# Performance work log

Hardware: AMD Instinct MI355X
Metric: run time of the kernel (lower is better)

## Reference

```python
import jax, jax.numpy as jnp
import numpy as np

B, S, T, D = 4, 512, 512, 256


def setup_inputs() -> dict:
    key = jax.random.key(0)
    ks = jax.random.split(key, 10)
    scale = 1.0 / np.sqrt(D)
    return {
        "source": jax.random.normal(ks[0], (B, S, D), jnp.float32),
        "target": jax.random.normal(ks[1], (B, T, D), jnp.float32),
        "W_src": jax.random.uniform(ks[2], (D, D), jnp.float32, -scale, scale),
        "b_src": jax.random.uniform(ks[3], (D,), jnp.float32, -scale, scale),
        "W_tgt": jax.random.uniform(ks[4], (D, D), jnp.float32, -scale, scale),
        "b_tgt": jax.random.uniform(ks[5], (D,), jnp.float32, -scale, scale),
        "W_res": jax.random.uniform(ks[6], (D, 1), jnp.float32, -scale, scale),
        "b_res": jax.random.uniform(ks[7], (1,), jnp.float32, -scale, scale),
        "W_prob": jax.random.uniform(ks[8], (D, 2), jnp.float32, -scale, scale),
        "b_prob": jax.random.uniform(ks[9], (2,), jnp.float32, -scale, scale),
    }


def reference(source, target, W_src, b_src, W_tgt, b_tgt, W_res, b_res, W_prob, b_prob):
    # source: (B,S,D), target: (B,T,D)
    src_lin = jnp.einsum("bsd,de->bse", source, W_src) + b_src  # (B,S,D)
    tgt_lin = jnp.einsum("btd,de->bte", target, W_tgt) + b_tgt  # (B,T,D)
    # Bahdanau-style additive attention: (B,T,S,D) broadcast, tanh, D->1
    h = jnp.tanh(src_lin[:, None, :, :] + tgt_lin[:, :, None, :])  # (B,T,S,D)
    genP = jnp.einsum("btsd,d->bts", h, W_res[:, 0]) + b_res[0]     # (B,T,S)
    prob = jax.nn.softmax(jnp.einsum("btd,de->bte", target, W_prob) + b_prob, axis=-1)  # (B,T,2)
    return genP, prob
```

## Files before the change

### kernel.cpp

```cpp
#include <hip/hip_runtime.h>

#define B_ 4
#define S_ 512
#define T_ 512
#define D_ 256
#define NSRC (B_ * S_)
#define NROW 4096
#define K2F 2.8853900817779268f

typedef __attribute__((ext_vector_type(8))) short short8;
typedef __attribute__((ext_vector_type(4))) float f32x4;
typedef __attribute__((ext_vector_type(2))) float f32x2;

__device__ __forceinline__ unsigned short f2bf(float f) {
    union { float f; unsigned u; } v; v.f = f;
    unsigned r = v.u + 0x7FFF + ((v.u >> 16) & 1);
    return (unsigned short)(r >> 16);
}

__global__ __launch_bounds__(256) void ysyt_kernel(
    const float* __restrict__ src, const float* __restrict__ tgt,
    const float* __restrict__ Wsrc, const float* __restrict__ Wtgt,
    const float* __restrict__ Wp,  const float* __restrict__ bp,
    const float* __restrict__ bsrc, const float* __restrict__ btgt,
    float* __restrict__ yst, float* __restrict__ out)
{
    __shared__ unsigned short lwt[16384];
    const int bid = blockIdx.x, tid = threadIdx.x;
    const int lane = tid & 63, w = tid >> 6;

    if (bid < 256) {
        const int rowblk = bid >> 2, colq = bid & 3;
        const int R0 = rowblk * 64;
        const int n = lane & 15, quad = lane >> 4;
        const int mat = (R0 >= NSRC) ? 1 : 0;
        const float* bias = mat ? btgt : bsrc;
        const float* Wm = mat ? Wtgt : Wsrc;
        const float* xb = mat ? &tgt[(R0 - NSRC) * D_] : &src[R0 * D_];

        {
            const int r = tid;
            const int ksr = r >> 5, qr = (r >> 3) & 3, jr = r & 7;
            const int wbase = ksr * 512 + qr * 8 + jr;
            #pragma unroll 4
            for (int i = 0; i < 16; i++) {
                float4 v = *(const float4*)&Wm[r * D_ + colq * 64 + 4 * i];
                const int cc = 4 * i;
                lwt[((cc + 0) >> 4) * 4096 + ((cc + 0) & 15) * 32 + wbase] = f2bf(v.x);
                lwt[((cc + 1) >> 4) * 4096 + ((cc + 1) & 15) * 32 + wbase] = f2bf(v.y);
                lwt[((cc + 2) >> 4) * 4096 + ((cc + 2) & 15) * 32 + wbase] = f2bf(v.z);
                lwt[((cc + 3) >> 4) * 4096 + ((cc + 3) & 15) * 32 + wbase] = f2bf(v.w);
            }
        }

        short8 af[8];
        #pragma unroll
        for (int ks = 0; ks < 8; ks++) {
            const float* p = &xb[(w * 16 + n) * D_ + ks * 32 + quad * 8];
            float4 u0 = *(const float4*)p;
            float4 u1 = *(const float4*)(p + 4);
            short8 v;
            v[0] = (short)f2bf(u0.x); v[1] = (short)f2bf(u0.y);
            v[2] = (short)f2bf(u0.z); v[3] = (short)f2bf(u0.w);
            v[4] = (short)f2bf(u1.x); v[5] = (short)f2bf(u1.y);
            v[6] = (short)f2bf(u1.z); v[7] = (short)f2bf(u1.w);
            af[ks] = v;
        }
        __syncthreads();

        #pragma unroll
        for (int gc = 0; gc < 4; gc++) {
            const int gcol = colq * 4 + gc;
            const unsigned short* bp2 = &lwt[gc * 4096 + n * 32 + quad * 8];
            short8 bf[8];
            #pragma unroll
            for (int ks = 0; ks < 8; ks++) bf[ks] = *(const short8*)&bp2[ks * 512];
            f32x4 a4 = {0.f, 0.f, 0.f, 0.f};
            #pragma unroll
            for (int ks = 0; ks < 8; ks++)
                a4 = __builtin_amdgcn_mfma_f32_16x16x32_bf16(af[ks], bf[ks], a4, 0, 0, 0);
            const float bv = bias[gcol * 16 + n];
            float4 o;
            o.x = __builtin_amdgcn_exp2f((a4[0] + bv) * K2F);
            o.y = __builtin_amdgcn_exp2f((a4[1] + bv) * K2F);
            o.z = __builtin_amdgcn_exp2f((a4[2] + bv) * K2F);
            o.w = __builtin_amdgcn_exp2f((a4[3] + bv) * K2F);
            *(float4*)&yst[(gcol * 16 + n) * NROW + R0 + w * 16 + quad * 4] = o;
        }
    } else {
        int row  = (bid - 256) * 4 + w;
        float p0 = 0.f, p1 = 0.f;
        #pragma unroll
        for (int i = 0; i < 4; i++) {
            int d = lane + i * 64;
            float v = tgt[row * D_ + d];
            float2 wv = *(const float2*)&Wp[d * 2];
            p0 = fmaf(v, wv.x, p0);
            p1 = fmaf(v, wv.y, p1);
        }
        #pragma unroll
        for (int off = 32; off > 0; off >>= 1) {
            p0 += __shfl_down(p0, off, 64);
            p1 += __shfl_down(p1, off, 64);
        }
        if (lane == 0) {
            const float L2E = 1.4426950408889634f;
            float l0 = p0 + bp[0], l1 = p1 + bp[1];
            float e10 = __builtin_amdgcn_exp2f((l1 - l0) * L2E);
            float e01 = __builtin_amdgcn_exp2f((l0 - l1) * L2E);
            out[B_ * T_ * S_ + row * 2 + 0] = __builtin_amdgcn_rcpf(1.f + e10);
            out[B_ * T_ * S_ + row * 2 + 1] = __builtin_amdgcn_rcpf(1.f + e01);
        }
    }
}

#define CLS 36
__global__ __launch_bounds__(256) void genp_kernel(
    const float* __restrict__ yst,
    const float* __restrict__ Wres, const float* __restrict__ bres,
    float* __restrict__ out)
{
    __shared__ float lys[2][64][CLS];
    __shared__ float lyt[2][64][CLS];
    __shared__ float c0s;

    const int tid = threadIdx.x;
    const int lane = tid & 63, w = tid >> 6;
    const int s0 = blockIdx.x * 32;
    const int t0 = blockIdx.y * 32;
    const int b  = blockIdx.z;
    const int m = tid & 15;
    const int g = tid >> 4;
    const int r = tid >> 3;
    const int q = tid & 7;

    if (w == 0) {
        float s = Wres[lane] + Wres[lane + 64] + Wres[lane + 128] + Wres[lane + 192];
        #pragma unroll
        for (int off = 32; off > 0; off >>= 1) s += __shfl_xor(s, off, 64);
        if (lane == 0) c0s = s + bres[0];
    }

    const int ysbase = b * S_ + s0;
    const int ytbase = NSRC + b * T_ + t0;

    {
        float4 a0 = *(const float4*)&yst[(r)      * NROW + ysbase + 4 * q];
        float4 a1 = *(const float4*)&yst[(r + 32) * NROW + ysbase + 4 * q];
        float4 b0 = *(const float4*)&yst[(r)      * NROW + ytbase + 4 * q];
        float4 b1 = *(const float4*)&yst[(r + 32) * NROW + ytbase + 4 * q];
        *(float4*)&lys[0][r][4 * q]      = a0;
        *(float4*)&lys[0][r + 32][4 * q] = a1;
        *(float4*)&lyt[0][r][4 * q]      = b0;
        *(float4*)&lyt[0][r + 32][4 * q] = b1;
    }
    __syncthreads();

    f32x2 acc[2];
    acc[0] = (f32x2){0.f, 0.f};
    acc[1] = (f32x2){0.f, 0.f};
    const f32x2 one2 = {1.f, 1.f};

    for (int c = 0; c < 4; c++) {
        const int bi = c & 1;
        float4 pa0, pa1, pb0, pb1;
        if (c < 3) {
            const int dn = (c + 1) * 64;
            pa0 = *(const float4*)&yst[(dn + r)      * NROW + ysbase + 4 * q];
            pa1 = *(const float4*)&yst[(dn + r + 32) * NROW + ysbase + 4 * q];
            pb0 = *(const float4*)&yst[(dn + r)      * NROW + ytbase + 4 * q];
            pb1 = *(const float4*)&yst[(dn + r + 32) * NROW + ytbase + 4 * q];
        }

        const float* wp = &Wres[c * 64];
        #pragma unroll 2
        for (int kq = 0; kq < 8; kq++) {
            const int d0 = 8 * kq;
            f32x2 ap[8];
            float2 ct[8];
            f32x2 wv[8];
            #pragma unroll
            for (int k = 0; k < 8; k++) {
                float2 a2 = *(const float2*)&lys[bi][d0 + k][2 * m];
                ct[k] = *(const float2*)&lyt[bi][d0 + k][2 * g];
                ap[k] = (f32x2){a2.x, a2.y};
                const float wk = wp[d0 + k];
                wv[k] = (f32x2){wk, wk};
            }
            #pragma unroll
            for (int i = 0; i < 2; i++) {
                const float c0 = i ? ct[0].y : ct[0].x;
                f32x2 dd[8];
                #pragma unroll
                for (int k = 0; k < 8; k++) {
                    const float cv = i ? ct[k].y : ct[k].x;
                    const f32x2 cs = {cv, cv};
                    dd[k] = ap[k] * cs + one2;
                }
                f32x2 p01 = dd[0] * dd[1];
                f32x2 p23 = dd[2] * dd[3];
                f32x2 p45 = dd[4] * dd[5];
                f32x2 p67 = dd[6] * dd[7];
                f32x2 q03 = p01 * p23;
                f32x2 q47 = p45 * p67;
                f32x2 den = q03 * q47;
                f32x2 u01 = dd[1] * wv[0]; u01 = dd[0] * wv[1] + u01;
                f32x2 u23 = dd[3] * wv[2]; u23 = dd[2] * wv[3] + u23;
                f32x2 u45 = dd[5] * wv[4]; u45 = dd[4] * wv[5] + u45;
                f32x2 u67 = dd[7] * wv[6]; u67 = dd[6] * wv[7] + u67;
                f32x2 n03 = u01 * p23; n03 = u23 * p01 + n03;
                f32x2 n47 = u45 * p67; n47 = u67 * p45 + n47;
                f32x2 num = n03 * q47; num = n47 * q03 + num;
                f32x2 rr;
                rr.x = __builtin_amdgcn_rcpf(den.x);
                rr.y = __builtin_amdgcn_rcpf(den.y);
                acc[i] = num * rr + acc[i];
                (void)c0;
            }
        }

        if (c < 3) {
            *(float4*)&lys[bi ^ 1][r][4 * q]      = pa0;
            *(float4*)&lys[bi ^ 1][r + 32][4 * q] = pa1;
            *(float4*)&lyt[bi ^ 1][r][4 * q]      = pb0;
            *(float4*)&lyt[bi ^ 1][r + 32][4 * q] = pb1;
        }
        __syncthreads();
    }

    const float C0 = c0s;
    #pragma unroll
    for (int i = 0; i < 2; i++) {
        float2 o;
        o.x = C0 - 2.f * acc[i].x;
        o.y = C0 - 2.f * acc[i].y;
        *(float2*)&out[(b * T_ + t0 + 2 * g + i) * S_ + s0 + 2 * m] = o;
    }
}

extern "C" void kernel_launch(void* const* d_in, const int* in_sizes, int n_in,
                              void* d_out, int out_size, void* d_ws, size_t ws_size,
                              hipStream_t stream) {
    const float* source = (const float*)d_in[0];
    const float* target = (const float*)d_in[1];
    const float* W_src  = (const float*)d_in[2];
    const float* b_src  = (const float*)d_in[3];
    const float* W_tgt  = (const float*)d_in[4];
    const float* b_tgt  = (const float*)d_in[5];
    const float* W_res  = (const float*)d_in[6];
    const float* b_res  = (const float*)d_in[7];
    const float* W_prob = (const float*)d_in[8];
    const float* b_prob = (const float*)d_in[9];
    float* out = (float*)d_out;

    float* yst = (float*)d_ws;

    ysyt_kernel<<<768, 256, 0, stream>>>(source, target, W_src, W_tgt,
                                         W_prob, b_prob, b_src, b_tgt,
                                         yst, out);
    genp_kernel<<<dim3(16, 16, 4), 256, 0, stream>>>(yst, W_res, b_res, out);
}
```

Baseline: 105.5 us.

## Split genP reduction over D halves, drop LDS staging, accumulate via atomics

The genP kernel no longer stages yst tiles through double-buffered shared memory. Each thread now loads its source and target columns straight from global memory into registers, with software prefetch. The D dimension is split across two blocks per batch, so each block covers 64 sources by 32 targets over half of D, and partial sums are combined with atomic adds into the output. The rational tanh product now groups 4 terms instead of 8, which roughly doubles the reciprocal count per element. The atomic accumulation also relies on the output being zeroed beforehand, and nothing visible in the launch code does that.

```diff
diff --git a/kernel.cpp b/kernel.cpp
--- a/kernel.cpp
+++ b/kernel.cpp
@@ -114,127 +114,104 @@
     }
 }
 
-#define CLS 36
 __global__ __launch_bounds__(256) void genp_kernel(
     const float* __restrict__ yst,
     const float* __restrict__ Wres, const float* __restrict__ bres,
     float* __restrict__ out)
 {
-    __shared__ float lys[2][64][CLS];
-    __shared__ float lyt[2][64][CLS];
-    __shared__ float c0s;
-
     const int tid = threadIdx.x;
-    const int lane = tid & 63, w = tid >> 6;
-    const int s0 = blockIdx.x * 32;
+    const int lane = tid & 63;
+    const int s0 = blockIdx.x * 64;
     const int t0 = blockIdx.y * 32;
-    const int b  = blockIdx.z;
-    const int m = tid & 15;
-    const int g = tid >> 4;
-    const int r = tid >> 3;
-    const int q = tid & 7;
-
-    if (w == 0) {
-        float s = Wres[lane] + Wres[lane + 64] + Wres[lane + 128] + Wres[lane + 192];
-        #pragma unroll
-        for (int off = 32; off > 0; off >>= 1) s += __shfl_xor(s, off, 64);
-        if (lane == 0) c0s = s + bres[0];
+    const int b  = blockIdx.z >> 1;
+    const int dh = blockIdx.z & 1;
+    const int m  = tid & 15;
+    const int g  = tid >> 4;
+
+    const int scol = b * S_ + s0 + 4 * m;
+    const int tcol = NSRC + b * T_ + t0 + 2 * g;
+    const int dbase = dh * 128;
+
+    f32x2 acc[2][2];
+    acc[0][0] = (f32x2){0.f, 0.f}; acc[0][1] = (f32x2){0.f, 0.f};
+    acc[1][0] = (f32x2){0.f, 0.f}; acc[1][1] = (f32x2){0.f, 0.f};
+    const f32x2 one2 = {1.f, 1.f};
+
+    #define KQLOAD(AS, AT, DQ) do {                                          \
+        _Pragma("unroll")                                                    \
+        for (int k = 0; k < 4; k++) {                                        \
+            AS[k] = *(const float4*)&yst[(size_t)((DQ) + k) * NROW + scol];  \
+            AT[k] = *(const float2*)&yst[(size_t)((DQ) + k) * NROW + tcol];  \
+        }                                                                    \
+    } while (0)
+
+    #define KQBODY(AS, AT, DQ) do {                                          \
+        const float w0 = Wres[(DQ) + 0], w1 = Wres[(DQ) + 1];                \
+        const float w2 = Wres[(DQ) + 2], w3 = Wres[(DQ) + 3];                \
+        const f32x2 wv0 = {w0, w0}, wv1 = {w1, w1};                          \
+        const f32x2 wv2 = {w2, w2}, wv3 = {w3, w3};                          \
+        _Pragma("unroll")                                                    \
+        for (int i = 0; i < 2; i++) {                                        \
+            const float c0 = i ? AT[0].y : AT[0].x;                          \
+            const float c1 = i ? AT[1].y : AT[1].x;                          \
+            const float c2 = i ? AT[2].y : AT[2].x;                          \
+            const float c3 = i ? AT[3].y : AT[3].x;                          \
+            const f32x2 c0v = {c0, c0}, c1v = {c1, c1};                      \
+            const f32x2 c2v = {c2, c2}, c3v = {c3, c3};                      \
+            _Pragma("unroll")                                                \
+            for (int jp = 0; jp < 2; jp++) {                                 \
+                const f32x2 a0 = jp ? (f32x2){AS[0].z, AS[0].w}              \
+                                    : (f32x2){AS[0].x, AS[0].y};             \
+                const f32x2 a1 = jp ? (f32x2){AS[1].z, AS[1].w}              \
+                                    : (f32x2){AS[1].x, AS[1].y};             \
+                const f32x2 a2 = jp ? (f32x2){AS[2].z, AS[2].w}              \
+                                    : (f32x2){AS[2].x, AS[2].y};             \
+                const f32x2 a3 = jp ? (f32x2){AS[3].z, AS[3].w}              \
+                                    : (f32x2){AS[3].x, AS[3].y};             \
+                f32x2 dd0 = a0 * c0v + one2;                                 \
+                f32x2 dd1 = a1 * c1v + one2;                                 \
+                f32x2 dd2 = a2 * c2v + one2;                                 \
+                f32x2 dd3 = a3 * c3v + one2;                                 \
+                f32x2 p01 = dd0 * dd1;                                       \
+                f32x2 p23 = dd2 * dd3;                                       \
+                f32x2 den = p01 * p23;                                       \
+                f32x2 u01 = dd1 * wv0; u01 = dd0 * wv1 + u01;                \
+                f32x2 u23 = dd3 * wv2; u23 = dd2 * wv3 + u23;                \
+                f32x2 num = u01 * p23; num = u23 * p01 + num;                \
+                f32x2 r;                                                     \
+                r.x = __builtin_amdgcn_rcpf(den.x);                          \
+                r.y = __builtin_amdgcn_rcpf(den.y);                          \
+                acc[i][jp] = num * r + acc[i][jp];                           \
+            }                                                                \
+        }                                                                    \
+    } while (0)
+
+    float4 sA[4], sB[4];
+    float2 tA[4], tB[4];
+    KQLOAD(sA, tA, dbase);
+    for (int it = 0; it < 16; it++) {
+        const int dq = dbase + it * 8;
+        KQLOAD(sB, tB, dq + 4);
+        KQBODY(sA, tA, dq);
+        if (it < 15) KQLOAD(sA, tA, dq + 8);
+        KQBODY(sB, tB, dq + 4);
     }
-
-    const int ysbase = b * S_ + s0;
-    const int ytbase = NSRC + b * T_ + t0;
-
-    {
-        float4 a0 = *(const float4*)&yst[(r)      * NROW + ysbase + 4 * q];
-        float4 a1 = *(const float4*)&yst[(r + 32) * NROW + ysbase + 4 * q];
-        float4 b0 = *(const float4*)&yst[(r)      * NROW + ytbase + 4 * q];
-        float4 b1 = *(const float4*)&yst[(r + 32) * NROW + ytbase + 4 * q];
-        *(float4*)&lys[0][r][4 * q]      = a0;
-        *(float4*)&lys[0][r + 32][4 * q] = a1;
-        *(float4*)&lyt[0][r][4 * q]      = b0;
-        *(float4*)&lyt[0][r + 32][4 * q] = b1;
-    }
-    __syncthreads();
-
-    f32x2 acc[2];
-    acc[0] = (f32x2){0.f, 0.f};
-    acc[1] = (f32x2){0.f, 0.f};
-    const f32x2 one2 = {1.f, 1.f};
-
-    for (int c = 0; c < 4; c++) {
-        const int bi = c & 1;
-        float4 pa0, pa1, pb0, pb1;
-        if (c < 3) {
-            const int dn = (c + 1) * 64;
-            pa0 = *(const float4*)&yst[(dn + r)      * NROW + ysbase + 4 * q];
-            pa1 = *(const float4*)&yst[(dn + r + 32) * NROW + ysbase + 4 * q];
-            pb0 = *(const float4*)&yst[(dn + r)      * NROW + ytbase + 4 * q];
-            pb1 = *(const float4*)&yst[(dn + r + 32) * NROW + ytbase + 4 * q];
-        }
-
-        const float* wp = &Wres[c * 64];
-        #pragma unroll 2
-        for (int kq = 0; kq < 8; kq++) {
-            const int d0 = 8 * kq;
-            f32x2 ap[8];
-            float2 ct[8];
-            f32x2 wv[8];
-            #pragma unroll
-            for (int k = 0; k < 8; k++) {
-                float2 a2 = *(const float2*)&lys[bi][d0 + k][2 * m];
-                ct[k] = *(const float2*)&lyt[bi][d0 + k][2 * g];
-                ap[k] = (f32x2){a2.x, a2.y};
-                const float wk = wp[d0 + k];
-                wv[k] = (f32x2){wk, wk};
-            }
-            #pragma unroll
-            for (int i = 0; i < 2; i++) {
-                const float c0 = i ? ct[0].y : ct[0].x;
-                f32x2 dd[8];
-                #pragma unroll
-                for (int k = 0; k < 8; k++) {
-                    const float cv = i ? ct[k].y : ct[k].x;
-                    const f32x2 cs = {cv, cv};
-                    dd[k] = ap[k] * cs + one2;
-                }
-                f32x2 p01 = dd[0] * dd[1];
-                f32x2 p23 = dd[2] * dd[3];
-                f32x2 p45 = dd[4] * dd[5];
-                f32x2 p67 = dd[6] * dd[7];
-                f32x2 q03 = p01 * p23;
-                f32x2 q47 = p45 * p67;
-                f32x2 den = q03 * q47;
-                f32x2 u01 = dd[1] * wv[0]; u01 = dd[0] * wv[1] + u01;
-                f32x2 u23 = dd[3] * wv[2]; u23 = dd[2] * wv[3] + u23;
-                f32x2 u45 = dd[5] * wv[4]; u45 = dd[4] * wv[5] + u45;
-                f32x2 u67 = dd[7] * wv[6]; u67 = dd[6] * wv[7] + u67;
-                f32x2 n03 = u01 * p23; n03 = u23 * p01 + n03;
-                f32x2 n47 = u45 * p67; n47 = u67 * p45 + n47;
-                f32x2 num = n03 * q47; num = n47 * q03 + num;
-                f32x2 rr;
-                rr.x = __builtin_amdgcn_rcpf(den.x);
-                rr.y = __builtin_amdgcn_rcpf(den.y);
-                acc[i] = num * rr + acc[i];
-                (void)c0;
-            }
-        }
-
-        if (c < 3) {
-            *(float4*)&lys[bi ^ 1][r][4 * q]      = pa0;
-            *(float4*)&lys[bi ^ 1][r + 32][4 * q] = pa1;
-            *(float4*)&lyt[bi ^ 1][r][4 * q]      = pb0;
-            *(float4*)&lyt[bi ^ 1][r + 32][4 * q] = pb1;
-        }
-        __syncthreads();
-    }
-
-    const float C0 = c0s;
+    #undef KQLOAD
+    #undef KQBODY
+
+    float cw = Wres[lane] + Wres[lane + 64] + Wres[lane + 128] + Wres[lane + 192];
+    #pragma unroll
+    for (int off = 32; off > 0; off >>= 1) cw += __shfl_xor(cw, off, 64);
+    const float C0 = (dh == 0) ? (cw + bres[0]) : 0.f;
+
     #pragma unroll
     for (int i = 0; i < 2; i++) {
-        float2 o;
-        o.x = C0 - 2.f * acc[i].x;
-        o.y = C0 - 2.f * acc[i].y;
-        *(float2*)&out[(b * T_ + t0 + 2 * g + i) * S_ + s0 + 2 * m] = o;
+        float* orow = &out[(size_t)(b * T_ + t0 + 2 * g + i) * S_ + s0 + 4 * m];
+        #pragma unroll
+        for (int jp = 0; jp < 2; jp++) {
+            unsafeAtomicAdd(&orow[2 * jp + 0], C0 - 2.f * acc[i][jp].x);
+            unsafeAtomicAdd(&orow[2 * jp + 1], C0 - 2.f * acc[i][jp].y);
+        }
     }
 }
 
@@ -258,5 +235,5 @@
     ysyt_kernel<<<768, 256, 0, stream>>>(source, target, W_src, W_tgt,
                                          W_prob, b_prob, b_src, b_tgt,
                                          yst, out);
-    genp_kernel<<<dim3(16, 16, 4), 256, 0, stream>>>(yst, W_res, b_res, out);
-}
+    genp_kernel<<<dim3(8, 16, 8), 256, 0, stream>>>(yst, W_res, b_res, out);
+}
```

Result: slower. 130.2 us (+23.4%).

## Store projected exponentials as row-major fp16 and read them as half8 in genp

Applied to the files above, without the earlier changes.

The projection kernel now stages its exp outputs in LDS, clamps them to 60000, converts them to fp16 and writes them row-major (row, D) instead of column-major fp32. The genp kernel loads half8 vectors along D, halving intermediate traffic and LDS footprint. It also remaps its thread-to-output tiling so that each thread handles rows m/m+16 and g/g+16. The risks are precision loss from fp16 storage and the clamp, plus an extra LDS pass and sync in the producer.

```diff
diff --git a/kernel.cpp b/kernel.cpp
--- a/kernel.cpp
+++ b/kernel.cpp
@@ -9,6 +9,7 @@
 #define K2F 2.8853900817779268f
 
 typedef __attribute__((ext_vector_type(8))) short short8;
+typedef __attribute__((ext_vector_type(8))) _Float16 half8;
 typedef __attribute__((ext_vector_type(4))) float f32x4;
 typedef __attribute__((ext_vector_type(2))) float f32x2;
 
@@ -23,9 +24,10 @@
     const float* __restrict__ Wsrc, const float* __restrict__ Wtgt,
     const float* __restrict__ Wp,  const float* __restrict__ bp,
     const float* __restrict__ bsrc, const float* __restrict__ btgt,
-    float* __restrict__ yst, float* __restrict__ out)
+    _Float16* __restrict__ ytr, float* __restrict__ out)
 {
     __shared__ unsigned short lwt[16384];
+    __shared__ _Float16 ltb[64][72];
     const int bid = blockIdx.x, tid = threadIdx.x;
     const int lane = tid & 63, w = tid >> 6;
 
@@ -80,12 +82,21 @@
             for (int ks = 0; ks < 8; ks++)
                 a4 = __builtin_amdgcn_mfma_f32_16x16x32_bf16(af[ks], bf[ks], a4, 0, 0, 0);
             const float bv = bias[gcol * 16 + n];
-            float4 o;
-            o.x = __builtin_amdgcn_exp2f((a4[0] + bv) * K2F);
-            o.y = __builtin_amdgcn_exp2f((a4[1] + bv) * K2F);
-            o.z = __builtin_amdgcn_exp2f((a4[2] + bv) * K2F);
-            o.w = __builtin_amdgcn_exp2f((a4[3] + bv) * K2F);
-            *(float4*)&yst[(gcol * 16 + n) * NROW + R0 + w * 16 + quad * 4] = o;
+            const int rl = w * 16 + quad * 4;
+            const int dl = gc * 16 + n;
+            ltb[rl + 0][dl] = (_Float16)fminf(__builtin_amdgcn_exp2f((a4[0] + bv) * K2F), 60000.f);
+            ltb[rl + 1][dl] = (_Float16)fminf(__builtin_amdgcn_exp2f((a4[1] + bv) * K2F), 60000.f);
+            ltb[rl + 2][dl] = (_Float16)fminf(__builtin_amdgcn_exp2f((a4[2] + bv) * K2F), 60000.f);
+            ltb[rl + 3][dl] = (_Float16)fminf(__builtin_amdgcn_exp2f((a4[3] + bv) * K2F), 60000.f);
+        }
+        __syncthreads();
+        {
+            const int row = tid >> 2, seg = tid & 3;
+            half8 v0 = *(const half8*)&ltb[row][seg * 16];
+            half8 v1 = *(const half8*)&ltb[row][seg * 16 + 8];
+            _Float16* dst = &ytr[(size_t)(R0 + row) * D_ + colq * 64 + seg * 16];
+            *(half8*)&dst[0] = v0;
+            *(half8*)&dst[8] = v1;
         }
     } else {
         int row  = (bid - 256) * 4 + w;
@@ -114,46 +125,31 @@
     }
 }
 
-#define CLS 36
 __global__ __launch_bounds__(256) void genp_kernel(
-    const float* __restrict__ yst,
+    const _Float16* __restrict__ ytr,
     const float* __restrict__ Wres, const float* __restrict__ bres,
     float* __restrict__ out)
 {
-    __shared__ float lys[2][64][CLS];
-    __shared__ float lyt[2][64][CLS];
-    __shared__ float c0s;
+    __shared__ _Float16 lys[2][32][72];
+    __shared__ _Float16 lyt[2][32][72];
 
     const int tid = threadIdx.x;
-    const int lane = tid & 63, w = tid >> 6;
+    const int lane = tid & 63;
     const int s0 = blockIdx.x * 32;
     const int t0 = blockIdx.y * 32;
     const int b  = blockIdx.z;
-    const int m = tid & 15;
-    const int g = tid >> 4;
-    const int r = tid >> 3;
-    const int q = tid & 7;
-
-    if (w == 0) {
-        float s = Wres[lane] + Wres[lane + 64] + Wres[lane + 128] + Wres[lane + 192];
-        #pragma unroll
-        for (int off = 32; off > 0; off >>= 1) s += __shfl_xor(s, off, 64);
-        if (lane == 0) c0s = s + bres[0];
-    }
-
-    const int ysbase = b * S_ + s0;
-    const int ytbase = NSRC + b * T_ + t0;
-
-    {
-        float4 a0 = *(const float4*)&yst[(r)      * NROW + ysbase + 4 * q];
-        float4 a1 = *(const float4*)&yst[(r + 32) * NROW + ysbase + 4 * q];
-        float4 b0 = *(const float4*)&yst[(r)      * NROW + ytbase + 4 * q];
-        float4 b1 = *(const float4*)&yst[(r + 32) * NROW + ytbase + 4 * q];
-        *(float4*)&lys[0][r][4 * q]      = a0;
-        *(float4*)&lys[0][r + 32][4 * q] = a1;
-        *(float4*)&lyt[0][r][4 * q]      = b0;
-        *(float4*)&lyt[0][r + 32][4 * q] = b1;
-    }
+    const int m  = tid & 15;
+    const int g  = tid >> 4;
+
+    const int srow = tid & 31;
+    const int sq   = (tid >> 5) & 7;
+    const size_t gsbase = (size_t)(b * S_ + s0 + srow) * D_;
+    const size_t gtbase = (size_t)(NSRC + b * T_ + t0 + srow) * D_;
+
+    half8 pvs = *(const half8*)&ytr[gsbase + 8 * sq];
+    half8 pvt = *(const half8*)&ytr[gtbase + 8 * sq];
+    *(half8*)&lys[0][srow][8 * sq] = pvs;
+    *(half8*)&lyt[0][srow][8 * sq] = pvt;
     __syncthreads();
 
     f32x2 acc[2];
@@ -163,79 +159,74 @@
 
     for (int c = 0; c < 4; c++) {
         const int bi = c & 1;
-        float4 pa0, pa1, pb0, pb1;
+        half8 nvs, nvt;
         if (c < 3) {
-            const int dn = (c + 1) * 64;
-            pa0 = *(const float4*)&yst[(dn + r)      * NROW + ysbase + 4 * q];
-            pa1 = *(const float4*)&yst[(dn + r + 32) * NROW + ysbase + 4 * q];
-            pb0 = *(const float4*)&yst[(dn + r)      * NROW + ytbase + 4 * q];
-            pb1 = *(const float4*)&yst[(dn + r + 32) * NROW + ytbase + 4 * q];
-        }
-
+            nvs = *(const half8*)&ytr[gsbase + (c + 1) * 64 + 8 * sq];
+            nvt = *(const half8*)&ytr[gtbase + (c + 1) * 64 + 8 * sq];
+        }
         const float* wp = &Wres[c * 64];
         #pragma unroll 2
         for (int kq = 0; kq < 8; kq++) {
-            const int d0 = 8 * kq;
-            f32x2 ap[8];
-            float2 ct[8];
+            half8 sL = *(const half8*)&lys[bi][m][8 * kq];
+            half8 sH = *(const half8*)&lys[bi][m + 16][8 * kq];
+            half8 tL = *(const half8*)&lyt[bi][g][8 * kq];
+            half8 tH = *(const half8*)&lyt[bi][g + 16][8 * kq];
+            f32x2 sp[8];
+            float tLf[8], tHf[8];
             f32x2 wv[8];
             #pragma unroll
             for (int k = 0; k < 8; k++) {
-                float2 a2 = *(const float2*)&lys[bi][d0 + k][2 * m];
-                ct[k] = *(const float2*)&lyt[bi][d0 + k][2 * g];
-                ap[k] = (f32x2){a2.x, a2.y};
-                const float wk = wp[d0 + k];
+                sp[k] = (f32x2){(float)sL[k], (float)sH[k]};
+                tLf[k] = (float)tL[k];
+                tHf[k] = (float)tH[k];
+                const float wk = wp[kq * 8 + k];
                 wv[k] = (f32x2){wk, wk};
             }
-            #pragma unroll
-            for (int i = 0; i < 2; i++) {
-                const float c0 = i ? ct[0].y : ct[0].x;
-                f32x2 dd[8];
-                #pragma unroll
-                for (int k = 0; k < 8; k++) {
-                    const float cv = i ? ct[k].y : ct[k].x;
-                    const f32x2 cs = {cv, cv};
-                    dd[k] = ap[k] * cs + one2;
-                }
-                f32x2 p01 = dd[0] * dd[1];
-                f32x2 p23 = dd[2] * dd[3];
-                f32x2 p45 = dd[4] * dd[5];
-                f32x2 p67 = dd[6] * dd[7];
-                f32x2 q03 = p01 * p23;
-                f32x2 q47 = p45 * p67;
-                f32x2 den = q03 * q47;
-                f32x2 u01 = dd[1] * wv[0]; u01 = dd[0] * wv[1] + u01;
-                f32x2 u23 = dd[3] * wv[2]; u23 = dd[2] * wv[3] + u23;
-                f32x2 u45 = dd[5] * wv[4]; u45 = dd[4] * wv[5] + u45;
-                f32x2 u67 = dd[7] * wv[6]; u67 = dd[6] * wv[7] + u67;
-                f32x2 n03 = u01 * p23; n03 = u23 * p01 + n03;
-                f32x2 n47 = u45 * p67; n47 = u67 * p45 + n47;
-                f32x2 num = n03 * q47; num = n47 * q03 + num;
-                f32x2 rr;
-                rr.x = __builtin_amdgcn_rcpf(den.x);
-                rr.y = __builtin_amdgcn_rcpf(den.y);
-                acc[i] = num * rr + acc[i];
-                (void)c0;
+            #define FOLD(TT, TF) {                                            \
+                f32x2 dd[8];                                                  \
+                _Pragma("unroll")                                             \
+                for (int k = 0; k < 8; k++) {                                 \
+                    const f32x2 cs2 = {TF[k], TF[k]};                         \
+                    dd[k] = sp[k] * cs2 + one2;                               \
+                }                                                             \
+                f32x2 p01 = dd[0] * dd[1];                                    \
+                f32x2 p23 = dd[2] * dd[3];                                    \
+                f32x2 p45 = dd[4] * dd[5];                                    \
+                f32x2 p67 = dd[6] * dd[7];                                    \
+                f32x2 q03 = p01 * p23;                                        \
+                f32x2 q47 = p45 * p67;                                        \
+                f32x2 den = q03 * q47;                                        \
+                f32x2 u01 = dd[1] * wv[0]; u01 = dd[0] * wv[1] + u01;         \
+                f32x2 u23 = dd[3] * wv[2]; u23 = dd[2] * wv[3] + u23;         \
+                f32x2 u45 = dd[5] * wv[4]; u45 = dd[4] * wv[5] + u45;         \
+                f32x2 u67 = dd[7] * wv[6]; u67 = dd[6] * wv[7] + u67;         \
+                f32x2 n03 = u01 * p23; n03 = u23 * p01 + n03;                 \
+                f32x2 n47 = u45 * p67; n47 = u67 * p45 + n47;                 \
+                f32x2 num = n03 * q47; num = n47 * q03 + num;                 \
+                f32x2 rr;                                                     \
+                rr.x = __builtin_amdgcn_rcpf(den.x);                          \
+                rr.y = __builtin_amdgcn_rcpf(den.y);                          \
+                acc[TT] = num * rr + acc[TT];                                 \
             }
-        }
-
+            FOLD(0, tLf) FOLD(1, tHf)
+            #undef FOLD
+        }
         if (c < 3) {
-            *(float4*)&lys[bi ^ 1][r][4 * q]      = pa0;
-            *(float4*)&lys[bi ^ 1][r + 32][4 * q] = pa1;
-            *(float4*)&lyt[bi ^ 1][r][4 * q]      = pb0;
-            *(float4*)&lyt[bi ^ 1][r + 32][4 * q] = pb1;
+            *(half8*)&lys[bi ^ 1][srow][8 * sq] = nvs;
+            *(half8*)&lyt[bi ^ 1][srow][8 * sq] = nvt;
         }
         __syncthreads();
     }
 
-    const float C0 = c0s;
+    float cw = Wres[lane] + Wres[lane + 64] + Wres[lane + 128] + Wres[lane + 192];
     #pragma unroll
-    for (int i = 0; i < 2; i++) {
-        float2 o;
-        o.x = C0 - 2.f * acc[i].x;
-        o.y = C0 - 2.f * acc[i].y;
-        *(float2*)&out[(b * T_ + t0 + 2 * g + i) * S_ + s0 + 2 * m] = o;
-    }
+    for (int off = 32; off > 0; off >>= 1) cw += __shfl_xor(cw, off, 64);
+    const float C0 = cw + bres[0];
+
+    out[(size_t)(b * T_ + t0 + g     ) * S_ + s0 + m     ] = C0 - 2.f * acc[0].x;
+    out[(size_t)(b * T_ + t0 + g     ) * S_ + s0 + m + 16] = C0 - 2.f * acc[0].y;
+    out[(size_t)(b * T_ + t0 + g + 16) * S_ + s0 + m     ] = C0 - 2.f * acc[1].x;
+    out[(size_t)(b * T_ + t0 + g + 16) * S_ + s0 + m + 16] = C0 - 2.f * acc[1].y;
 }
 
 extern "C" void kernel_launch(void* const* d_in, const int* in_sizes, int n_in,
@@ -253,10 +244,10 @@
     const float* b_prob = (const float*)d_in[9];
     float* out = (float*)d_out;
 
-    float* yst = (float*)d_ws;
+    _Float16* ytr = (_Float16*)d_ws;
 
     ysyt_kernel<<<768, 256, 0, stream>>>(source, target, W_src, W_tgt,
                                          W_prob, b_prob, b_src, b_tgt,
-                                         yst, out);
-    genp_kernel<<<dim3(16, 16, 4), 256, 0, stream>>>(yst, W_res, b_res, out);
-}
+                                         ytr, out);
+    genp_kernel<<<dim3(16, 16, 4), 256, 0, stream>>>(ytr, W_res, b_res, out);
+}
```

Measured after the change: 108.4 us. +2.8%, slower.
